# Optimization experiments

Measured on AMD Instinct MI355X. Metric: run time of the kernel, lower is better.

Reference implementation:

```python
import jax, jax.numpy as jnp
import numpy as np

ANCHORS = np.array([[10., 13.], [16., 30.], [33., 23.]], dtype=np.float32)
NUM_CLASSES = 80
IMG_W, IMG_H = 416, 416
IGNORE_THR = 0.5
OBJ_SCALE, NOOBJ_SCALE = 1.0, 0.5
EPS = 1e-12


def setup_inputs() -> dict:
    key = jax.random.key(0)
    k1, k2, k3, k4, k5 = jax.random.split(key, 5)
    B, A, C, H, W = 16, 3, NUM_CLASSES, 52, 52
    x = jax.random.normal(k1, (B, A * (C + 5), H, W), dtype=jnp.float32)
    N = 256
    img = jax.random.randint(k2, (N,), 0, B).astype(jnp.float32)
    xy = jax.random.uniform(k3, (N, 2), minval=0.02, maxval=0.98, dtype=jnp.float32)
    wh = jax.random.uniform(k4, (N, 2), minval=0.02, maxval=0.5, dtype=jnp.float32)
    cls = jax.random.randint(k5, (N,), 0, C).astype(jnp.float32)
    target = jnp.concatenate([img[:, None], xy, wh, cls[:, None]], axis=1)
    return {"x": x, "target": target}


def _masked_mse(p, t, m):
    n = jnp.maximum(jnp.sum(m), 1.0)
    return jnp.sum(m * (p - t) ** 2) / n


def _masked_bce(p, t, m):
    p = jnp.clip(p, EPS, 1.0 - EPS)
    n = jnp.maximum(jnp.sum(m), 1.0)
    return jnp.sum(m * (-(t * jnp.log(p) + (1.0 - t) * jnp.log(1.0 - p)))) / n


def _yolo(x, target):
    anchors = jnp.asarray(ANCHORS)
    B, A, C = x.shape[0], anchors.shape[0], NUM_CLASSES
    H, W = x.shape[2], x.shape[3]
    stride_h, stride_w = IMG_H / H, IMG_W / W
    # [B, A, H, W, C+5]
    pred = x.reshape(B, A, C + 5, H, W).transpose(0, 1, 3, 4, 2)
    cx = jax.nn.sigmoid(pred[..., 0])
    cy = jax.nn.sigmoid(pred[..., 1])
    pw = pred[..., 2]
    ph = pred[..., 3]
    pconf = jax.nn.sigmoid(pred[..., 4])
    pcls = jax.nn.sigmoid(pred[..., 5:])

    # ---- detect (boxes use .data in torch -> stop_gradient) ----
    grid_x = jnp.arange(W, dtype=jnp.float32)[None, None, None, :]
    grid_y = jnp.arange(H, dtype=jnp.float32)[None, None, :, None]
    scale_aw = (anchors[:, 0] / stride_w).reshape(1, A, 1, 1)
    scale_ah = (anchors[:, 1] / stride_h).reshape(1, A, 1, 1)
    bx = jax.lax.stop_gradient(cx) + grid_x
    by = jax.lax.stop_gradient(cy) + grid_y
    bw = jnp.exp(jax.lax.stop_gradient(pw)) * scale_aw
    bh = jnp.exp(jax.lax.stop_gradient(ph)) * scale_ah
    boxes = jnp.stack([bx * stride_w, by * stride_h, bw * stride_w, bh * stride_h], -1)
    output = jnp.concatenate(
        [boxes.reshape(B, -1, 4), pconf.reshape(B, -1, 1), pcls.reshape(B, -1, C)], -1)

    # ---- build targets ----
    img_num = target[:, 0].astype(jnp.int32)
    gxc = target[:, 1] * W
    gyc = target[:, 2] * H
    gw = target[:, 3] * W
    gh = target[:, 4] * H
    label = target[:, 5].astype(jnp.int32)
    # wh-IoU of raw pixel anchors vs grid-unit gt (faithful to original, which
    # passes unscaled self.anchors to bbox_wh_iou)
    aw = anchors[:, 0][:, None]  # [A,1]
    ah = anchors[:, 1][:, None]
    inter = jnp.minimum(aw, gw[None, :]) * jnp.minimum(ah, gh[None, :])
    ious = inter / (aw * ah + 1e-16 + gw[None, :] * gh[None, :] - inter)  # [A,N]
    best_index = jnp.argmax(ious, axis=0)  # [N]
    gi = gxc.astype(jnp.int32)
    gj = gyc.astype(jnp.int32)

    shp = (B, A, H, W)
    obj_mask = jnp.zeros(shp, jnp.float32).at[img_num, best_index, gj, gi].set(1.0)
    noobj_mask = jnp.ones(shp, jnp.float32).at[img_num, best_index, gj, gi].set(0.0)
    # zero noobj where any anchor IoU > ignore threshold
    N = target.shape[0]
    anc = jnp.broadcast_to(jnp.arange(A, dtype=jnp.int32)[:, None], (A, N))
    img_b = jnp.broadcast_to(img_num[None, :], (A, N))
    gj_b = jnp.broadcast_to(gj[None, :], (A, N))
    gi_b = jnp.broadcast_to(gi[None, :], (A, N))
    keep = jnp.where(ious > IGNORE_THR, 0.0, 1.0)
    noobj_mask = noobj_mask.at[img_b, anc, gj_b, gi_b].min(keep)

    tx = jnp.zeros(shp, jnp.float32).at[img_num, best_index, gj, gi].set(gxc - jnp.floor(gxc))
    ty = jnp.zeros(shp, jnp.float32).at[img_num, best_index, gj, gi].set(gyc - jnp.floor(gyc))
    tw = jnp.zeros(shp, jnp.float32).at[img_num, best_index, gj, gi].set(
        jnp.log(gw / anchors[best_index, 0] + 1e-16))
    th = jnp.zeros(shp, jnp.float32).at[img_num, best_index, gj, gi].set(
        jnp.log(gh / anchors[best_index, 1] + 1e-16))
    tconf = jnp.zeros(shp, jnp.float32).at[img_num, best_index, gj, gi].set(1.0)
    tcls = jnp.zeros(shp + (C,), jnp.float32).at[img_num, best_index, gj, gi, label].set(1.0)

    # ---- masked losses (replicating original's center_x/self.w bugs) ----
    loss_x = _masked_mse(cx, tx, obj_mask)
    loss_y = _masked_mse(cx, ty, obj_mask)   # original uses center_x for y loss
    loss_w = _masked_mse(pw, tw, obj_mask)
    loss_h = _masked_mse(pw, th, obj_mask)   # original uses self.w for h loss
    loss_conf = (OBJ_SCALE * _masked_bce(pconf, tconf, obj_mask)
                 + NOOBJ_SCALE * _masked_bce(pconf, tconf, noobj_mask))
    cls_mask = jnp.broadcast_to(obj_mask[..., None], tcls.shape)
    loss_cls = _masked_bce(pcls, tcls, cls_mask)
    total = loss_x + loss_y + loss_w + loss_h + loss_conf + loss_cls
    return output, total


def reference(x, target):
    return _yolo(x, target)
```

## Files before the change

### kernel.cpp

```cpp
#include <hip/hip_runtime.h>
#include <math.h>

#define NA 3
#define NC 80
#define CH 85
#define NB 16
#define HH 52
#define WW 52
#define HW 2704
#define HWF4 676
#define NT 256
#define NCELLS (NB*NA*HW)
#define NBMW 4056
#define STRIDE_F 8.0f
#define IGN_THR 0.5f

#define TF4 26
#define NF4 2210
#define LSTR 105
#define LDSW 8945
#define NDENSE 1248
#define NDSL 1023
#define NTILE2 225
#define WIN_D0 955
#define ZERO_D0 1019
#define TAIL_DEND 1022
#define GRID 1024

#define SW(c, l) ((c) * LSTR + (l) + ((c) >> 2))

__device__ __forceinline__ float sigm(float z) { return 1.0f / (1.0f + expf(-z)); }
__device__ __forceinline__ float splus(float z) { return log1pf(expf(z)); }


__global__ __launch_bounds__(256) void yolo_one(
        const float* __restrict__ x, float* __restrict__ out,
        const float* __restrict__ target, float* acc, int* cnts,
        int* wofs, float* wtx, float* wty, float* wtw, float* wth,
        int* wlabel, int* zofs, float* __restrict__ out_total) {
    __shared__ float lds[LDSW];
    __shared__ float red[4];
    __shared__ int s_flag[2];
    int bid = blockIdx.x;
    int t = threadIdx.x;

    if (bid == 0) {
        unsigned int* bm = (unsigned int*)lds;
        int* s_keyobj = (int*)lds + NBMW;
        int* s_cnt = (int*)lds + NBMW + NT;
        if (t == 0) { s_cnt[0] = 0; s_cnt[1] = 0; }
        for (int i = t; i < NBMW; i += 256) bm[i] = 0u;

        const float awc[3] = {10.f, 16.f, 33.f};
        const float ahc[3] = {13.f, 30.f, 23.f};
        float timg = target[t*6 + 0];
        float gxc  = target[t*6 + 1] * (float)WW;
        float gyc  = target[t*6 + 2] * (float)HH;
        float gw   = target[t*6 + 3] * (float)WW;
        float gh   = target[t*6 + 4] * (float)HH;
        int label  = (int)target[t*6 + 5];

        float best_iou = -1.0f;
        int best = 0, ignbits = 0;
        for (int a = 0; a < 3; a++) {
            float inter = fminf(awc[a], gw) * fminf(ahc[a], gh);
            float iou = inter / (awc[a]*ahc[a] + 1e-16f + gw*gh - inter);
            if (iou > best_iou) { best_iou = iou; best = a; }
            if (iou > IGN_THR) ignbits |= (1 << a);
        }
        int img = (int)timg;
        int gi = (int)gxc, gj = (int)gyc;
        int pixel = gj * WW + gi;
        int cellbase = img * (NA * HW) + pixel;
        int keyobj = cellbase + best * HW;
        s_keyobj[t] = keyobj;
        __syncthreads();

        bool dup = false;
        #pragma unroll 8
        for (int m = 0; m < NT; m++) {
            int k = s_keyobj[m];
            dup = dup || (m > t && k == keyobj);
        }
        int sink = 0;
        if (!dup) {
            int p = atomicAdd(&s_cnt[0], 1);
            sink ^= atomicExch(&wofs[p], (img * NA + best) * (CH * HW) + pixel);
            sink ^= __float_as_int(atomicExch(&wtx[p], gxc - floorf(gxc)));
            sink ^= __float_as_int(atomicExch(&wty[p], gyc - floorf(gyc)));
            sink ^= __float_as_int(atomicExch(&wtw[p], logf(gw / awc[best] + 1e-16f)));
            sink ^= __float_as_int(atomicExch(&wth[p], logf(gh / ahc[best] + 1e-16f)));
            sink ^= atomicExch(&wlabel[p], label);
        }
        for (int a = 0; a < 3; a++) {
            bool flag = (a == best) || ((ignbits >> a) & 1);
            if (flag) {
                int key = cellbase + a * HW;
                unsigned int bit = 1u << (key & 31);
                unsigned int old = atomicOr(&bm[key >> 5], bit);
                if (!(old & bit)) {
                    int p = atomicAdd(&s_cnt[1], 1);
                    sink ^= atomicExch(&zofs[p],
                                ((img * NA + a) * CH + 4) * HW + pixel);
                }
            }
        }
        asm volatile("" :: "v"(sink) : "memory");
        __syncthreads();
        if (t == 0) {
            int o0 = atomicExch(&cnts[0], s_cnt[0]);
            int o1 = atomicExch(&cnts[1], s_cnt[1]);
            asm volatile("" :: "v"(o0), "v"(o1) : "memory");
            int of = atomicExch(&cnts[4], 1);
            asm volatile("" :: "v"(of) : "memory");
            int o = atomicAdd(&cnts[3], 1);
            if (o == GRID - 1) {
                float a0 = atomicAdd(&acc[0], 0.0f);
                float a1 = atomicAdd(&acc[1], 0.0f);
                float a2 = atomicAdd(&acc[2], 0.0f);
                float a3 = atomicAdd(&acc[3], 0.0f);
                float wc = (float)atomicAdd(&cnts[0], 0);
                float zc = (float)atomicAdd(&cnts[1], 0);
                float n_obj = fmaxf(wc, 1.0f);
                float n_noobj = fmaxf((float)NCELLS - zc, 1.0f);
                float cls_den = fmaxf(80.0f * wc, 1.0f);
                out_total[0] = a1 / n_obj + a2 / cls_den
                             + 0.5f * ((a0 - a3) / n_noobj);
            }
        }
        return;
    }

    int d = bid - 1;
    const float awc[3] = {10.f, 16.f, 33.f};
    const float ahc[3] = {13.f, 30.f, 23.f};
    float blk_noobj = 0.0f;
    int ntiles = (d < NTILE2) ? 2 : 1;
    for (int it = 0; it < ntiles; it++) {
        int dtile = (it == 0) ? d : d + NDSL;
        if (it) __syncthreads();
        int chunk = dtile % 26;
        int ba    = dtile / 26;
        int a     = ba % NA;

        const float4* x4 = (const float4*)x + (size_t)ba * (CH * HWF4)
                                            + chunk * TF4;
        float4 v[9];
        #pragma unroll
        for (int i = 0; i < 9; i++) {
            int idx = t + i * 256;
            if (idx < NF4) {
                int c = idx / TF4, q = idx - c * TF4;
                v[i] = x4[c * HWF4 + q];
            }
        }
        float noobj = 0.0f;
        #pragma unroll
        for (int i = 0; i < 9; i++) {
            int idx = t + i * 256;
            if (idx < NF4) {
                int c = idx / TF4, q = idx - c * TF4;
                float r[4] = {v[i].x, v[i].y, v[i].z, v[i].w};
                #pragma unroll
                for (int k = 0; k < 4; k++) {
                    int l = q * 4 + k;
                    float z = r[k], o;
                    if (c == 0) {
                        int wc = l - ((l >= WW) ? WW : 0);
                        o = (sigm(z) + (float)wc) * STRIDE_F;
                    } else if (c == 1) {
                        int hc = chunk * 2 + ((l >= WW) ? 1 : 0);
                        o = (sigm(z) + (float)hc) * STRIDE_F;
                    } else if (c == 2) {
                        o = expf(z) * awc[a];
                    } else if (c == 3) {
                        o = expf(z) * ahc[a];
                    } else {
                        o = sigm(z);
                        if (c == 4) noobj += splus(z);
                    }
                    lds[SW(c, l)] = o;
                }
            }
        }
        for (int off = 32; off > 0; off >>= 1)
            noobj += __shfl_down(noobj, off, 64);
        if ((t & 63) == 0) red[t >> 6] = noobj;
        __syncthreads();

        float4* o4 = (float4*)out + (size_t)ba * (HW * CH / 4) + chunk * NF4;
        #pragma unroll
        for (int i = 0; i < 9; i++) {
            int j = t + i * 256;
            if (j < NF4) {
                int flat = 4 * j;
                int cell = flat / CH;
                int ch = flat - cell * CH;
                float4 w;
                float* pw = &w.x;
                #pragma unroll
                for (int k = 0; k < 4; k++) {
                    int chk = ch + k, cek = cell;
                    if (chk >= CH) { chk -= CH; cek += 1; }
                    pw[k] = lds[SW(chk, cek)];
                }
                o4[j] = w;
            }
        }
        if (t == 0) blk_noobj += red[0] + red[1] + red[2] + red[3];
    }

    if (d >= WIN_D0 && d < TAIL_DEND) {
        if (t == 0) {
            while (atomicAdd(&cnts[4], 0) == 0)
                __builtin_amdgcn_s_sleep(8);
            s_flag[0] = atomicAdd(&cnts[0], 0);
            s_flag[1] = atomicAdd(&cnts[1], 0);
        }
        __syncthreads();

        if (d < ZERO_D0) {
            int wave = t >> 6, lane = t & 63;
            int w = (d - WIN_D0) * 4 + wave;
            if (w < s_flag[0]) {
                int ofs = 0, label = 0;
                float ttx = 0.f, tty = 0.f, ttw = 0.f, tth = 0.f;
                if (lane == 0) {
                    ofs   = atomicAdd(&wofs[w], 0);
                    label = atomicAdd(&wlabel[w], 0);
                    ttx = atomicAdd(&wtx[w], 0.0f);
                    tty = atomicAdd(&wty[w], 0.0f);
                    ttw = atomicAdd(&wtw[w], 0.0f);
                    tth = atomicAdd(&wth[w], 0.0f);
                }
                ofs   = __shfl(ofs, 0, 64);
                label = __shfl(label, 0, 64);
                const float* xp = x + ofs;
                float lcls;
                {
                    float z = xp[(size_t)(5 + lane) * HW];
                    lcls = (lane == label) ? splus(-z) : splus(z);
                }
                if (lane < 16) {
                    int c = 64 + lane;
                    float z = xp[(size_t)(5 + c) * HW];
                    lcls += (c == label) ? splus(-z) : splus(z);
                }
                float other = 0.0f;
                if (lane == 0) {
                    float z0 = xp[0];
                    float z2 = xp[(size_t)2 * HW];
                    float z4 = xp[(size_t)4 * HW];
                    float cx = sigm(z0);
                    float dx = cx - ttx, dy = cx - tty;
                    float dw = z2 - ttw, dh = z2 - tth;
                    other = dx*dx + dy*dy + dw*dw + dh*dh + splus(-z4);
                }
                for (int off = 32; off > 0; off >>= 1)
                    lcls += __shfl_down(lcls, off, 64);
                if (lane == 0) {
                    float o1 = atomicAdd(&acc[1], other);
                    float o2 = atomicAdd(&acc[2], lcls);
                    asm volatile("" :: "v"(o1), "v"(o2) : "memory");
                }
            }
        } else {
            int idx = (d - ZERO_D0) * 256 + t;
            float vv = 0.0f;
            if (idx < s_flag[1]) {
                int z = atomicAdd(&zofs[idx], 0);
                vv = splus(x[z]);
            }
            for (int off = 32; off > 0; off >>= 1)
                vv += __shfl_down(vv, off, 64);
            if ((t & 63) == 0) {
                float o3 = atomicAdd(&acc[3], vv);
                asm volatile("" :: "v"(o3) : "memory");
            }
        }
        __syncthreads();
    }

    if (t == 0) {
        float old = atomicAdd(&acc[0], blk_noobj);
        asm volatile("" :: "v"(old) : "memory");
        int o = atomicAdd(&cnts[3], 1);
        if (o == GRID - 1) {
            float a0 = atomicAdd(&acc[0], 0.0f);
            float a1 = atomicAdd(&acc[1], 0.0f);
            float a2 = atomicAdd(&acc[2], 0.0f);
            float a3 = atomicAdd(&acc[3], 0.0f);
            float wc = (float)atomicAdd(&cnts[0], 0);
            float zc = (float)atomicAdd(&cnts[1], 0);
            float n_obj = fmaxf(wc, 1.0f);
            float n_noobj = fmaxf((float)NCELLS - zc, 1.0f);
            float cls_den = fmaxf(80.0f * wc, 1.0f);
            out_total[0] = a1 / n_obj + a2 / cls_den
                         + 0.5f * ((a0 - a3) / n_noobj);
        }
    }
}

extern "C" void kernel_launch(void* const* d_in, const int* in_sizes, int n_in,
                              void* d_out, int out_size, void* d_ws, size_t ws_size,
                              hipStream_t stream) {
    (void)in_sizes; (void)n_in; (void)out_size; (void)ws_size;
    const float* x      = (const float*)d_in[0];
    const float* target = (const float*)d_in[1];
    float* out = (float*)d_out;

    char* ws = (char*)d_ws;
    float* acc      = (float*)(ws + 0);
    int*   cnts     = (int*)  (ws + 64);
    int*   wofs     = (int*)  (ws + 128);
    float* wtx      = (float*)(ws + 1152);
    float* wty      = (float*)(ws + 2176);
    float* wtw      = (float*)(ws + 3200);
    float* wth      = (float*)(ws + 4224);
    int*   wlabel   = (int*)  (ws + 5248);
    int*   zofs     = (int*)  (ws + 6272);

    hipMemsetAsync(ws, 0, 96, stream);
    yolo_one<<<GRID, 256, 0, stream>>>(
        x, out, target, acc, cnts, wofs, wtx, wty, wtw, wth, wlabel, zofs,
        out + (size_t)NB * NA * HW * CH);
}
```

Measured before the change: 127.9 us.

## Move transpose to per-wave 16-cell tiles with register double-buffered prefetch

Restructures the dense transpose-and-activate phase so each wave independently handles 16-cell tiles in its own LDS slice, synchronising with wave barriers instead of block-wide __syncthreads. The next tile's loads are issued into a second register set while the current tile is computed and stored. Work is redistributed across a smaller grid of 513 blocks, with the first 67 blocks doing short epilogue-sized tile runs before waiting on the target-build flag. Per-wave noobj partials are atomically added directly instead of being reduced per block. The narrow 16-cell tiles produce shorter contiguous reads per channel row, and the extra register buffers raise register pressure.

```diff
diff --git a/kernel.cpp b/kernel.cpp
--- a/kernel.cpp
+++ b/kernel.cpp
@@ -15,19 +15,19 @@
 #define STRIDE_F 8.0f
 #define IGN_THR 0.5f
 
-#define TF4 26
-#define NF4 2210
-#define LSTR 105
-#define LDSW 8945
-#define NDENSE 1248
-#define NDSL 1023
-#define NTILE2 225
-#define WIN_D0 955
-#define ZERO_D0 1019
-#define TAIL_DEND 1022
-#define GRID 1024
-
-#define SW(c, l) ((c) * LSTR + (l) + ((c) >> 2))
+#define NTPLANE 169
+#define NWTILES (NTPLANE*NB*NA)
+#define S2 86
+#define WLDS (16*S2)
+#define NF4C 340
+
+#define NEPIB 67
+#define NEPIW (NEPIB*4)
+#define EPITILES (NEPIW*2)
+#define NNORMB 445
+#define NNW (NNORMB*4)
+#define NREM 456
+#define GRID (1 + NEPIB + NNORMB)
 
 __device__ __forceinline__ float sigm(float z) { return 1.0f / (1.0f + expf(-z)); }
 __device__ __forceinline__ float splus(float z) { return log1pf(expf(z)); }
@@ -38,8 +38,7 @@
         const float* __restrict__ target, float* acc, int* cnts,
         int* wofs, float* wtx, float* wty, float* wtw, float* wth,
         int* wlabel, int* zofs, float* __restrict__ out_total) {
-    __shared__ float lds[LDSW];
-    __shared__ float red[4];
+    __shared__ float lds[4 * WLDS];
     __shared__ int s_flag[2];
     int bid = blockIdx.x;
     int t = threadIdx.x;
@@ -131,46 +130,67 @@
         return;
     }
 
+    int wave = t >> 6, lane = t & 63;
     int d = bid - 1;
+    float* wl = &lds[wave * WLDS];
     const float awc[3] = {10.f, 16.f, 33.f};
     const float ahc[3] = {13.f, 30.f, 23.f};
-    float blk_noobj = 0.0f;
-    int ntiles = (d < NTILE2) ? 2 : 1;
-    for (int it = 0; it < ntiles; it++) {
-        int dtile = (it == 0) ? d : d + NDSL;
-        if (it) __syncthreads();
-        int chunk = dtile % 26;
-        int ba    = dtile / 26;
-        int a     = ba % NA;
-
-        const float4* x4 = (const float4*)x + (size_t)ba * (CH * HWF4)
-                                            + chunk * TF4;
-        float4 v[9];
+
+    int wt, tStride, tCount;
+    if (d < NEPIB) {
+        int ew = d * 4 + wave;
+        wt = ew * 2; tStride = 1; tCount = 2;
+    } else {
+        int nw = (d - NEPIB) * 4 + wave;
+        wt = EPITILES + nw; tStride = NNW;
+        tCount = 4 + (nw < NREM ? 1 : 0);
+    }
+
+    float noobj = 0.0f;
+    float4 vc[6], vn[6];
+    {
+        int ba_ = wt / NTPLANE, tp_ = wt - ba_ * NTPLANE;
+        const float4* p_ = (const float4*)x + (size_t)ba_ * (CH * HWF4)
+                                            + tp_ * 4 + (lane & 3);
         #pragma unroll
-        for (int i = 0; i < 9; i++) {
-            int idx = t + i * 256;
-            if (idx < NF4) {
-                int c = idx / TF4, q = idx - c * TF4;
-                v[i] = x4[c * HWF4 + q];
-            }
-        }
-        float noobj = 0.0f;
+        for (int i = 0; i < 6; i++) {
+            int c = i * 16 + (lane >> 2);
+            if (c < CH) vc[i] = p_[(size_t)c * HWF4];
+        }
+    }
+    for (int it = 0; it < tCount; it++) {
+        bool hasnext = (it + 1 < tCount);
+        int nwt = wt + tStride;
+        if (hasnext) {
+            int ba_ = nwt / NTPLANE, tp_ = nwt - ba_ * NTPLANE;
+            const float4* p_ = (const float4*)x
+                + (size_t)ba_ * (CH * HWF4) + tp_ * 4 + (lane & 3);
+            #pragma unroll
+            for (int i = 0; i < 6; i++) {
+                int c = i * 16 + (lane >> 2);
+                if (c < CH) vn[i] = p_[(size_t)c * HWF4];
+            }
+        }
+        int ba = wt / NTPLANE, tp = wt - ba * NTPLANE;
+        int a = ba % NA;
+
         #pragma unroll
-        for (int i = 0; i < 9; i++) {
-            int idx = t + i * 256;
-            if (idx < NF4) {
-                int c = idx / TF4, q = idx - c * TF4;
-                float r[4] = {v[i].x, v[i].y, v[i].z, v[i].w};
+        for (int i = 0; i < 6; i++) {
+            int c = i * 16 + (lane >> 2);
+            if (c < CH) {
+                float r[4] = {vc[i].x, vc[i].y, vc[i].z, vc[i].w};
                 #pragma unroll
                 for (int k = 0; k < 4; k++) {
-                    int l = q * 4 + k;
+                    int cell = 4 * (lane & 3) + k;
                     float z = r[k], o;
                     if (c == 0) {
-                        int wc = l - ((l >= WW) ? WW : 0);
-                        o = (sigm(z) + (float)wc) * STRIDE_F;
+                        int gp = tp * 16 + cell;
+                        int px = gp % WW;
+                        o = (sigm(z) + (float)px) * STRIDE_F;
                     } else if (c == 1) {
-                        int hc = chunk * 2 + ((l >= WW) ? 1 : 0);
-                        o = (sigm(z) + (float)hc) * STRIDE_F;
+                        int gp = tp * 16 + cell;
+                        int py = gp / WW;
+                        o = (sigm(z) + (float)py) * STRIDE_F;
                     } else if (c == 2) {
                         o = expf(z) * awc[a];
                     } else if (c == 3) {
@@ -179,38 +199,47 @@
                         o = sigm(z);
                         if (c == 4) noobj += splus(z);
                     }
-                    lds[SW(c, l)] = o;
-                }
-            }
-        }
-        for (int off = 32; off > 0; off >>= 1)
-            noobj += __shfl_down(noobj, off, 64);
-        if ((t & 63) == 0) red[t >> 6] = noobj;
-        __syncthreads();
-
-        float4* o4 = (float4*)out + (size_t)ba * (HW * CH / 4) + chunk * NF4;
+                    wl[cell * S2 + c] = o;
+                }
+            }
+        }
+        __builtin_amdgcn_wave_barrier();
+
+        float4* o4 = (float4*)out + (size_t)ba * (HW * CH / 4) + tp * NF4C;
         #pragma unroll
-        for (int i = 0; i < 9; i++) {
-            int j = t + i * 256;
-            if (j < NF4) {
+        for (int i = 0; i < 6; i++) {
+            int j = lane + i * 64;
+            if (j < NF4C) {
                 int flat = 4 * j;
-                int cell = flat / CH;
-                int ch = flat - cell * CH;
+                int ce = flat / CH;
+                int c0 = flat - ce * CH;
                 float4 w;
                 float* pw = &w.x;
                 #pragma unroll
                 for (int k = 0; k < 4; k++) {
-                    int chk = ch + k, cek = cell;
-                    if (chk >= CH) { chk -= CH; cek += 1; }
-                    pw[k] = lds[SW(chk, cek)];
+                    int ch = c0 + k, cek = ce;
+                    if (ch >= CH) { ch -= CH; cek += 1; }
+                    pw[k] = wl[cek * S2 + ch];
                 }
                 o4[j] = w;
             }
         }
-        if (t == 0) blk_noobj += red[0] + red[1] + red[2] + red[3];
-    }
-
-    if (d >= WIN_D0 && d < TAIL_DEND) {
+        __builtin_amdgcn_wave_barrier();
+
+        if (hasnext) {
+            #pragma unroll
+            for (int i = 0; i < 6; i++) vc[i] = vn[i];
+        }
+        wt = nwt;
+    }
+    for (int off = 32; off > 0; off >>= 1)
+        noobj += __shfl_down(noobj, off, 64);
+    if (lane == 0) {
+        float old = atomicAdd(&acc[0], noobj);
+        asm volatile("" :: "v"(old) : "memory");
+    }
+
+    if (d < NEPIB) {
         if (t == 0) {
             while (atomicAdd(&cnts[4], 0) == 0)
                 __builtin_amdgcn_s_sleep(8);
@@ -219,9 +248,8 @@
         }
         __syncthreads();
 
-        if (d < ZERO_D0) {
-            int wave = t >> 6, lane = t & 63;
-            int w = (d - WIN_D0) * 4 + wave;
+        if (d < 64) {
+            int w = d * 4 + wave;
             if (w < s_flag[0]) {
                 int ofs = 0, label = 0;
                 float ttx = 0.f, tty = 0.f, ttw = 0.f, tth = 0.f;
@@ -265,7 +293,7 @@
                 }
             }
         } else {
-            int idx = (d - ZERO_D0) * 256 + t;
+            int idx = (d - 64) * 256 + t;
             float vv = 0.0f;
             if (idx < s_flag[1]) {
                 int z = atomicAdd(&zofs[idx], 0);
@@ -278,12 +306,10 @@
                 asm volatile("" :: "v"(o3) : "memory");
             }
         }
-        __syncthreads();
-    }
-
+    }
+
+    __syncthreads();
     if (t == 0) {
-        float old = atomicAdd(&acc[0], blk_noobj);
-        asm volatile("" :: "v"(old) : "memory");
         int o = atomicAdd(&cnts[3], 1);
         if (o == GRID - 1) {
             float a0 = atomicAdd(&acc[0], 0.0f);
```

After: 142.5 us. +11.4%, slower.

## Use persistent blocks with atomic tile queue and register double-buffered prefetch

Applied to the files above, without the earlier changes.

The grid shrinks from 1024 to 513 blocks. The dense blocks become persistent workers that take tiles from an atomic counter and prefetch the next tile's global loads into a second register buffer while the current tile is written out. The sparse object and zero-offset tail work is folded into the first 67 workers after their first tile. LDS barriers become raw s_barrier calls with explicit waitcnt. The aim is to hide load latency and cut block launch overhead, at the cost of higher register pressure (two float4[9] buffers), which may reduce occupancy, plus per-tile atomic contention on the queue counter.

```diff
diff --git a/kernel.cpp b/kernel.cpp
--- a/kernel.cpp
+++ b/kernel.cpp
@@ -20,18 +20,44 @@
 #define LSTR 105
 #define LDSW 8945
 #define NDENSE 1248
-#define NDSL 1023
-#define NTILE2 225
-#define WIN_D0 955
-#define ZERO_D0 1019
-#define TAIL_DEND 1022
-#define GRID 1024
+#define NDB 512
+#define NEPI 67
+#define GRID (1 + NDB)
 
 #define SW(c, l) ((c) * LSTR + (l) + ((c) >> 2))
 
 __device__ __forceinline__ float sigm(float z) { return 1.0f / (1.0f + expf(-z)); }
 __device__ __forceinline__ float splus(float z) { return log1pf(expf(z)); }
 
+
+__device__ __forceinline__ void load_tile(const float* __restrict__ x,
+                                          int dtile, int t, float4 (&v)[9]) {
+    int chunk = dtile % 26, ba = dtile / 26;
+    const float4* x4 = (const float4*)x + (size_t)ba * (CH * HWF4)
+                                        + chunk * TF4;
+    #pragma unroll
+    for (int i = 0; i < 9; i++) {
+        int idx = t + i * 256;
+        if (idx < NF4) {
+            int c = idx / TF4, q = idx - c * TF4;
+            v[i] = x4[c * HWF4 + q];
+        }
+    }
+}
+
+__device__ __forceinline__ void finalize_total(float* acc, int* cnts,
+                                               float* out_total) {
+    float a0 = atomicAdd(&acc[0], 0.0f);
+    float a1 = atomicAdd(&acc[1], 0.0f);
+    float a2 = atomicAdd(&acc[2], 0.0f);
+    float a3 = atomicAdd(&acc[3], 0.0f);
+    float wc = (float)atomicAdd(&cnts[0], 0);
+    float zc = (float)atomicAdd(&cnts[1], 0);
+    float n_obj = fmaxf(wc, 1.0f);
+    float n_noobj = fmaxf((float)NCELLS - zc, 1.0f);
+    float cls_den = fmaxf(80.0f * wc, 1.0f);
+    out_total[0] = a1 / n_obj + a2 / cls_den + 0.5f * ((a0 - a3) / n_noobj);
+}
 
 __global__ __launch_bounds__(256) void yolo_one(
         const float* __restrict__ x, float* __restrict__ out,
@@ -40,6 +66,7 @@
         int* wlabel, int* zofs, float* __restrict__ out_total) {
     __shared__ float lds[LDSW];
     __shared__ float red[4];
+    __shared__ int s_nt[2];
     __shared__ int s_flag[2];
     int bid = blockIdx.x;
     int t = threadIdx.x;
@@ -114,19 +141,7 @@
             int of = atomicExch(&cnts[4], 1);
             asm volatile("" :: "v"(of) : "memory");
             int o = atomicAdd(&cnts[3], 1);
-            if (o == GRID - 1) {
-                float a0 = atomicAdd(&acc[0], 0.0f);
-                float a1 = atomicAdd(&acc[1], 0.0f);
-                float a2 = atomicAdd(&acc[2], 0.0f);
-                float a3 = atomicAdd(&acc[3], 0.0f);
-                float wc = (float)atomicAdd(&cnts[0], 0);
-                float zc = (float)atomicAdd(&cnts[1], 0);
-                float n_obj = fmaxf(wc, 1.0f);
-                float n_noobj = fmaxf((float)NCELLS - zc, 1.0f);
-                float cls_den = fmaxf(80.0f * wc, 1.0f);
-                out_total[0] = a1 / n_obj + a2 / cls_den
-                             + 0.5f * ((a0 - a3) / n_noobj);
-            }
+            if (o == GRID - 1) finalize_total(acc, cnts, out_total);
         }
         return;
     }
@@ -134,27 +149,21 @@
     int d = bid - 1;
     const float awc[3] = {10.f, 16.f, 33.f};
     const float ahc[3] = {13.f, 30.f, 23.f};
-    float blk_noobj = 0.0f;
-    int ntiles = (d < NTILE2) ? 2 : 1;
-    for (int it = 0; it < ntiles; it++) {
-        int dtile = (it == 0) ? d : d + NDSL;
-        if (it) __syncthreads();
-        int chunk = dtile % 26;
-        int ba    = dtile / 26;
+
+    if (t == 0) s_nt[0] = atomicAdd(&cnts[5], 1);
+    __syncthreads();
+    int cur = s_nt[0];
+    int par = 0;
+    float4 v[9], vn[9];
+    if (cur < NDENSE) load_tile(x, cur, t, v);
+    int until_tail = (d < NEPI) ? 1 : -1;
+    float noobj = 0.0f;
+
+    while (cur < NDENSE) {
+        if (t == 0) s_nt[par ^ 1] = atomicAdd(&cnts[5], 1);
+        int chunk = cur % 26;
+        int ba    = cur / 26;
         int a     = ba % NA;
-
-        const float4* x4 = (const float4*)x + (size_t)ba * (CH * HWF4)
-                                            + chunk * TF4;
-        float4 v[9];
-        #pragma unroll
-        for (int i = 0; i < 9; i++) {
-            int idx = t + i * 256;
-            if (idx < NF4) {
-                int c = idx / TF4, q = idx - c * TF4;
-                v[i] = x4[c * HWF4 + q];
-            }
-        }
-        float noobj = 0.0f;
         #pragma unroll
         for (int i = 0; i < 9; i++) {
             int idx = t + i * 256;
@@ -183,10 +192,12 @@
                 }
             }
         }
-        for (int off = 32; off > 0; off >>= 1)
-            noobj += __shfl_down(noobj, off, 64);
-        if ((t & 63) == 0) red[t >> 6] = noobj;
-        __syncthreads();
+        asm volatile("s_waitcnt lgkmcnt(0)" ::: "memory");
+        __builtin_amdgcn_s_barrier();
+        __builtin_amdgcn_sched_barrier(0);
+
+        int nt = s_nt[par ^ 1];
+        if (nt < NDENSE) load_tile(x, nt, t, vn);
 
         float4* o4 = (float4*)out + (size_t)ba * (HW * CH / 4) + chunk * NF4;
         #pragma unroll
@@ -207,97 +218,95 @@
                 o4[j] = w;
             }
         }
-        if (t == 0) blk_noobj += red[0] + red[1] + red[2] + red[3];
+        asm volatile("s_waitcnt lgkmcnt(0)" ::: "memory");
+        __builtin_amdgcn_s_barrier();
+        __builtin_amdgcn_sched_barrier(0);
+
+        #pragma unroll
+        for (int i = 0; i < 9; i++) v[i] = vn[i];
+        cur = nt;
+        par ^= 1;
+
+        if (until_tail > 0 && --until_tail == 0) {
+            if (t == 0) {
+                while (atomicAdd(&cnts[4], 0) == 0)
+                    __builtin_amdgcn_s_sleep(8);
+                s_flag[0] = atomicAdd(&cnts[0], 0);
+                s_flag[1] = atomicAdd(&cnts[1], 0);
+            }
+            __syncthreads();
+            int wave = t >> 6, lane = t & 63;
+            if (d < 64) {
+                int w = d * 4 + wave;
+                if (w < s_flag[0]) {
+                    int ofs = 0, label = 0;
+                    float ttx = 0.f, tty = 0.f, ttw = 0.f, tth = 0.f;
+                    if (lane == 0) {
+                        ofs   = atomicAdd(&wofs[w], 0);
+                        label = atomicAdd(&wlabel[w], 0);
+                        ttx = atomicAdd(&wtx[w], 0.0f);
+                        tty = atomicAdd(&wty[w], 0.0f);
+                        ttw = atomicAdd(&wtw[w], 0.0f);
+                        tth = atomicAdd(&wth[w], 0.0f);
+                    }
+                    ofs   = __shfl(ofs, 0, 64);
+                    label = __shfl(label, 0, 64);
+                    const float* xp = x + ofs;
+                    float lcls;
+                    {
+                        float z = xp[(size_t)(5 + lane) * HW];
+                        lcls = (lane == label) ? splus(-z) : splus(z);
+                    }
+                    if (lane < 16) {
+                        int c = 64 + lane;
+                        float z = xp[(size_t)(5 + c) * HW];
+                        lcls += (c == label) ? splus(-z) : splus(z);
+                    }
+                    float other = 0.0f;
+                    if (lane == 0) {
+                        float z0 = xp[0];
+                        float z2 = xp[(size_t)2 * HW];
+                        float z4 = xp[(size_t)4 * HW];
+                        float cx = sigm(z0);
+                        float dx = cx - ttx, dy = cx - tty;
+                        float dw = z2 - ttw, dh = z2 - tth;
+                        other = dx*dx + dy*dy + dw*dw + dh*dh + splus(-z4);
+                    }
+                    for (int off = 32; off > 0; off >>= 1)
+                        lcls += __shfl_down(lcls, off, 64);
+                    if (lane == 0) {
+                        float o1 = atomicAdd(&acc[1], other);
+                        float o2 = atomicAdd(&acc[2], lcls);
+                        asm volatile("" :: "v"(o1), "v"(o2) : "memory");
+                    }
+                }
+            } else {
+                int idx = (d - 64) * 256 + t;
+                float vv = 0.0f;
+                if (idx < s_flag[1]) {
+                    int z = atomicAdd(&zofs[idx], 0);
+                    vv = splus(x[z]);
+                }
+                for (int off = 32; off > 0; off >>= 1)
+                    vv += __shfl_down(vv, off, 64);
+                if ((t & 63) == 0) {
+                    float o3 = atomicAdd(&acc[3], vv);
+                    asm volatile("" :: "v"(o3) : "memory");
+                }
+            }
+            __syncthreads();
+        }
     }
 
-    if (d >= WIN_D0 && d < TAIL_DEND) {
-        if (t == 0) {
-            while (atomicAdd(&cnts[4], 0) == 0)
-                __builtin_amdgcn_s_sleep(8);
-            s_flag[0] = atomicAdd(&cnts[0], 0);
-            s_flag[1] = atomicAdd(&cnts[1], 0);
-        }
-        __syncthreads();
-
-        if (d < ZERO_D0) {
-            int wave = t >> 6, lane = t & 63;
-            int w = (d - WIN_D0) * 4 + wave;
-            if (w < s_flag[0]) {
-                int ofs = 0, label = 0;
-                float ttx = 0.f, tty = 0.f, ttw = 0.f, tth = 0.f;
-                if (lane == 0) {
-                    ofs   = atomicAdd(&wofs[w], 0);
-                    label = atomicAdd(&wlabel[w], 0);
-                    ttx = atomicAdd(&wtx[w], 0.0f);
-                    tty = atomicAdd(&wty[w], 0.0f);
-                    ttw = atomicAdd(&wtw[w], 0.0f);
-                    tth = atomicAdd(&wth[w], 0.0f);
-                }
-                ofs   = __shfl(ofs, 0, 64);
-                label = __shfl(label, 0, 64);
-                const float* xp = x + ofs;
-                float lcls;
-                {
-                    float z = xp[(size_t)(5 + lane) * HW];
-                    lcls = (lane == label) ? splus(-z) : splus(z);
-                }
-                if (lane < 16) {
-                    int c = 64 + lane;
-                    float z = xp[(size_t)(5 + c) * HW];
-                    lcls += (c == label) ? splus(-z) : splus(z);
-                }
-                float other = 0.0f;
-                if (lane == 0) {
-                    float z0 = xp[0];
-                    float z2 = xp[(size_t)2 * HW];
-                    float z4 = xp[(size_t)4 * HW];
-                    float cx = sigm(z0);
-                    float dx = cx - ttx, dy = cx - tty;
-                    float dw = z2 - ttw, dh = z2 - tth;
-                    other = dx*dx + dy*dy + dw*dw + dh*dh + splus(-z4);
-                }
-                for (int off = 32; off > 0; off >>= 1)
-                    lcls += __shfl_down(lcls, off, 64);
-                if (lane == 0) {
-                    float o1 = atomicAdd(&acc[1], other);
-                    float o2 = atomicAdd(&acc[2], lcls);
-                    asm volatile("" :: "v"(o1), "v"(o2) : "memory");
-                }
-            }
-        } else {
-            int idx = (d - ZERO_D0) * 256 + t;
-            float vv = 0.0f;
-            if (idx < s_flag[1]) {
-                int z = atomicAdd(&zofs[idx], 0);
-                vv = splus(x[z]);
-            }
-            for (int off = 32; off > 0; off >>= 1)
-                vv += __shfl_down(vv, off, 64);
-            if ((t & 63) == 0) {
-                float o3 = atomicAdd(&acc[3], vv);
-                asm volatile("" :: "v"(o3) : "memory");
-            }
-        }
-        __syncthreads();
-    }
-
+    for (int off = 32; off > 0; off >>= 1)
+        noobj += __shfl_down(noobj, off, 64);
+    if ((t & 63) == 0) red[t >> 6] = noobj;
+    __syncthreads();
     if (t == 0) {
-        float old = atomicAdd(&acc[0], blk_noobj);
+        float old = atomicAdd(&acc[0], red[0] + red[1] + red[2] + red[3]);
         asm volatile("" :: "v"(old) : "memory");
         int o = atomicAdd(&cnts[3], 1);
-        if (o == GRID - 1) {
-            float a0 = atomicAdd(&acc[0], 0.0f);
-            float a1 = atomicAdd(&acc[1], 0.0f);
-            float a2 = atomicAdd(&acc[2], 0.0f);
-            float a3 = atomicAdd(&acc[3], 0.0f);
-            float wc = (float)atomicAdd(&cnts[0], 0);
-            float zc = (float)atomicAdd(&cnts[1], 0);
-            float n_obj = fmaxf(wc, 1.0f);
-            float n_noobj = fmaxf((float)NCELLS - zc, 1.0f);
-            float cls_den = fmaxf(80.0f * wc, 1.0f);
-            out_total[0] = a1 / n_obj + a2 / cls_den
-                         + 0.5f * ((a0 - a3) / n_noobj);
-        }
+        if (o == GRID - 1) finalize_total(acc, cnts, out_total);
     }
 }
 
```

Result: slower. 179.3 us (+40.2%).
